# Performance work log

Hardware: AMD Instinct MI355X
Metric: run time of the kernel (lower is better)

Reference implementation:

```python
import jax, jax.numpy as jnp
import numpy as np

N_NODES = 50000
N_EDGES = 800000
NEG_SLOPE = 0.2


def _gat_layer(x, src, dst, W, a_src, a_dst, bias, heads, out_ch):
    """PyG-style GATConv with self-loops already appended to src/dst."""
    N = x.shape[0]
    h = (x @ W.T).reshape(N, heads, out_ch)            # [N,H,C]
    alpha_src = jnp.einsum('nhc,hc->nh', h, a_src)      # [N,H]
    alpha_dst = jnp.einsum('nhc,hc->nh', h, a_dst)      # [N,H]
    e = jax.nn.leaky_relu(alpha_src[src] + alpha_dst[dst], NEG_SLOPE)  # [E,H]
    # segment softmax over incoming edges of each destination node
    m = jax.ops.segment_max(e, dst, num_segments=N)     # [N,H]
    ex = jnp.exp(e - m[dst])
    denom = jax.ops.segment_sum(ex, dst, num_segments=N)  # [N,H] (>0: self-loops)
    alpha = ex / (denom[dst] + 1e-16)                    # [E,H]
    out = jax.ops.segment_sum(h[src] * alpha[:, :, None], dst, num_segments=N)  # [N,H,C]
    return out.reshape(N, heads * out_ch) + bias


def _with_self_loops(edge_index, n):
    loop = jnp.arange(n, dtype=edge_index.dtype)
    src = jnp.concatenate([edge_index[0], loop])
    dst = jnp.concatenate([edge_index[1], loop])
    return src, dst


def setup_inputs() -> dict:
    key = jax.random.key(0)
    ks = jax.random.split(key, 12)
    s = lambda fan: 1.0 / np.sqrt(fan)
    return {
        'x': jax.random.normal(ks[0], (N_NODES, 16), jnp.float32),
        'edge_index': jax.random.randint(ks[1], (2, N_EDGES), 0, N_NODES, jnp.int64),
        'W1': jax.random.normal(ks[2], (256, 16), jnp.float32) * s(16),
        'att_src1': jax.random.normal(ks[3], (4, 64), jnp.float32) * s(64),
        'att_dst1': jax.random.normal(ks[4], (4, 64), jnp.float32) * s(64),
        'b1': jnp.zeros((256,), jnp.float32),
        'W2': jax.random.normal(ks[5], (64, 256), jnp.float32) * s(256),
        'att_src2': jax.random.normal(ks[6], (1, 64), jnp.float32) * s(64),
        'att_dst2': jax.random.normal(ks[7], (1, 64), jnp.float32) * s(64),
        'b2': jnp.zeros((64,), jnp.float32),
        'fc_w': jax.random.normal(ks[8], (1, 64), jnp.float32) * s(64),
        'fc_b': jnp.zeros((1,), jnp.float32),
    }


def reference(x, edge_index, W1, att_src1, att_dst1, b1,
              W2, att_src2, att_dst2, b2, fc_w, fc_b):
    src, dst = _with_self_loops(edge_index, x.shape[0])
    h = jax.nn.elu(_gat_layer(x, src, dst, W1, att_src1, att_dst1, b1, heads=4, out_ch=64))
    h = jax.nn.elu(_gat_layer(h, src, dst, W2, att_src2, att_dst2, b2, heads=1, out_ch=64))
    return h @ fc_w.T + fc_b
```

## Files before the change

kernel.cpp:

```cpp
#include <hip/hip_runtime.h>
#include <hip/hip_bf16.h>
#include <stdint.h>

#define N_NODES 50000
#define N_EDGES 800000
#define MAXDEG  96
#define NSLICE  6250
#define NSB     196

#define OFF_X    0
#define OFF_W1   800000
#define OFF_AS1  804096
#define OFF_AD1  804352
#define OFF_B1   804608
#define OFF_W2   804864
#define OFF_AS2  821248
#define OFF_AD2  821312
#define OFF_B2   821376
#define OFF_FCW  821440
#define OFF_FCB  821504
#define N_CANON  821505
#define N_W2B    16384
#define N_W1B    16384
#define N_CONV   (N_CANON + N_W2B + N_W1B + N_NODES)

typedef __hip_bfloat16 bf16;
typedef __attribute__((ext_vector_type(8))) short short8;
typedef __attribute__((ext_vector_type(4))) float f32x4;

__device__ __forceinline__ float b2f(bf16 v){ return (float)v; }
__device__ __forceinline__ int clampi(int v, int lo, int hi){ return v < lo ? lo : (v > hi ? hi : v); }
__device__ __forceinline__ float clampf(float v){ return fminf(fmaxf(v, -40.f), 40.f); }
__device__ __forceinline__ uint16_t f2bfbits(float f){
  union { float f; uint32_t u; } c; c.f = f;
  uint32_t r = c.u + 0x7fff + ((c.u >> 16) & 1);
  return (uint16_t)(r >> 16);
}
__device__ __forceinline__ float bitsf(uint32_t u){
  union { uint32_t u; float f; } c; c.u = u; return c.f;
}
__device__ __forceinline__ uint32_t fbits(float f){
  union { float f; uint32_t u; } c; c.f = f; return c.u;
}

__device__ __forceinline__ int load_src(const int* ei, int i, int f){
  return f ? ei[2*(size_t)i] : ei[i];
}
__device__ __forceinline__ int load_dst(const int* ei, int i, int f){
  return f ? ei[2*((size_t)N_EDGES + i)] : ei[N_EDGES + i];
}

__global__ void k_detect(const int* __restrict__ ei, const uint16_t* __restrict__ xu,
                         int* __restrict__ flag){
  const int l = threadIdx.x;
  int or_odd = ei[2*l + 1] | ei[2*(400000 + l) + 1];
  int hits = 0;
  for(int k = 0; k < 64; k++){
    int e = (xu[l*64 + k] >> 7) & 0xFF;
    hits += (e >= 200);
  }
  #pragma unroll
  for(int off=32; off; off>>=1){
    or_odd |= __shfl_xor(or_odd, off, 64);
    hits   += __shfl_xor(hits,   off, 64);
  }
  if(l == 0){
    flag[0] = (or_odd == 0) ? 1 : 0;
    flag[1] = (hits > 16) ? 1 : 0;
  }
}

__global__ void k_convert(const void* x, const void* W1, const void* as1w, const void* ad1w,
                          const void* b1, const void* W2, const void* as2w, const void* ad2w,
                          const void* b2, const void* fcw, const void* fcb,
                          float* __restrict__ canon, uint16_t* __restrict__ W2b,
                          uint16_t* __restrict__ W1b, int* __restrict__ cnt,
                          int* __restrict__ csr_pad, const int* __restrict__ flag){
  int i = blockIdx.x*256 + threadIdx.x;
  int fp32 = flag[1];
  if(i >= N_CANON + N_W2B + N_W1B){
    int j = i - (N_CANON + N_W2B + N_W1B);
    if(j < N_NODES){ cnt[j] = 1; csr_pad[(size_t)j*MAXDEG] = j; }
    return;
  }
  if(i >= N_CANON + N_W2B){
    int j2 = i - (N_CANON + N_W2B);
    int j = j2 >> 6, kk = j2 & 63;
    uint16_t v = 0;
    if((kk >> 4) == (j >> 6)){
      int e = j*16 + (kk & 15);
      v = fp32 ? f2bfbits(((const float*)W1)[e]) : ((const uint16_t*)W1)[e];
    }
    W1b[j2] = v;
    return;
  }
  if(i >= N_CANON){
    int j = i - N_CANON;
    W2b[j] = fp32 ? f2bfbits(((const float*)W2)[j]) : ((const uint16_t*)W2)[j];
    return;
  }
  const void* src; int off;
  if     (i < OFF_W1 ){ src = x;    off = i; }
  else if(i < OFF_AS1){ src = W1;   off = i - OFF_W1; }
  else if(i < OFF_AD1){ src = as1w; off = i - OFF_AS1; }
  else if(i < OFF_B1 ){ src = ad1w; off = i - OFF_AD1; }
  else if(i < OFF_W2 ){ src = b1;   off = i - OFF_B1; }
  else if(i < OFF_AS2){ src = W2;   off = i - OFF_W2; }
  else if(i < OFF_AD2){ src = as2w; off = i - OFF_AS2; }
  else if(i < OFF_B2 ){ src = ad2w; off = i - OFF_AD2; }
  else if(i < OFF_FCW){ src = b2;   off = i - OFF_B2; }
  else if(i < OFF_FCB){ src = fcw;  off = i - OFF_FCW; }
  else               { src = fcb;  off = 0; }
  float v = fp32 ? ((const float*)src)[off] : b2f(((const bf16*)src)[off]);
  canon[i] = v;
}


__global__ __launch_bounds__(256) void k_prepscat(const float* __restrict__ canon,
                        uint32_t* __restrict__ pack, float* __restrict__ dpack,
                        const int* __restrict__ ei, int* __restrict__ cnt,
                        int* __restrict__ csr_pad, const int* __restrict__ flag){
  const int tid = threadIdx.x;
  if(blockIdx.x >= 196){
    const int bid = blockIdx.x - 196;
    const int grp = bid & 7, sb = bid >> 3;
    const int f = flag[0];
    const int lo = grp*NSLICE, hi = lo + NSLICE;
    const int base = sb*4096;
    #pragma unroll 4
    for(int j = 0; j < 16; j++){
      int i = base + j*256 + tid;
      if(i >= N_EDGES) break;
      int d = clampi(load_dst(ei, i, f), 0, N_NODES-1);
      if(d >= lo && d < hi){
        int s = clampi(load_src(ei, i, f), 0, N_NODES-1);
        int pos = atomicAdd(&cnt[d], 1);
        pos = clampi(pos, 0, MAXDEG-1);
        csr_pad[(size_t)d*MAXDEG + pos] = s;
      }
    }
    return;
  }
  __shared__ float ps[64], pd[64];
  if(tid < 128){
    int e = tid & 63;
    int h = e >> 4, k = e & 15;
    const float* av = canon + (tid < 64 ? OFF_AS1 : OFF_AD1) + h*64;
    const float* Wp = canon + OFF_W1 + (h*64)*16 + k;
    float acc = 0.f;
    #pragma unroll 8
    for(int c = 0; c < 64; c++) acc += av[c] * Wp[c*16];
    (tid < 64 ? ps : pd)[e] = acc;
  }
  __syncthreads();
  int n = blockIdx.x*256 + tid;
  if(n >= N_NODES) return;
  float xr[16];
  const float4* xp = (const float4*)(canon + OFF_X + n*16);
  #pragma unroll
  for(int t=0;t<4;t++){ float4 v = xp[t]; xr[4*t]=v.x; xr[4*t+1]=v.y; xr[4*t+2]=v.z; xr[4*t+3]=v.w; }
  uint32_t w[16];
  #pragma unroll
  for(int t=0;t<8;t++)
    w[t] = (uint32_t)f2bfbits(xr[2*t]) | ((uint32_t)f2bfbits(xr[2*t+1]) << 16);
  float qs[8];
  #pragma unroll
  for(int h=0;h<4;h++){
    float a=0.f, b=0.f;
    #pragma unroll
    for(int k=0;k<16;k++){ a += ps[h*16+k]*xr[k]; b += pd[h*16+k]*xr[k]; }
    a = clampf(a); b = clampf(b);
    w[8+2*h]  = fbits(__expf(a));
    w[9+2*h]  = fbits(__expf(0.2f*a));
    qs[2*h]   = __expf(b);
    qs[2*h+1] = __expf(0.2f*b);
  }
  uint4* dst = (uint4*)(pack + (size_t)n*16);
  dst[0] = make_uint4(w[0],w[1],w[2],w[3]);
  dst[1] = make_uint4(w[4],w[5],w[6],w[7]);
  dst[2] = make_uint4(w[8],w[9],w[10],w[11]);
  dst[3] = make_uint4(w[12],w[13],w[14],w[15]);
  float4* dd = (float4*)(dpack + (size_t)n*8);
  dd[0] = make_float4(qs[0],qs[1],qs[2],qs[3]);
  dd[1] = make_float4(qs[4],qs[5],qs[6],qs[7]);
}


struct Acc { float y0,y1,y2,y3,d0,d1,d2,d3; };

__device__ __forceinline__ void batch8(const int* __restrict__ csr, int i0, const char* pk,
                                       float2 qq, int g, int k, int h3, int base, Acc& a){
  int iA = csr[i0 + g], iB = csr[i0 + 4 + g];
  const char* rA = pk + (size_t)iA*64;
  const char* rB = pk + (size_t)iB*64;
  float xvA = bitsf((uint32_t)(*(const uint16_t*)(rA + k*2)) << 16);
  float2 ppA = *(const float2*)(rA + 32 + h3*8);
  float xvB = bitsf((uint32_t)(*(const uint16_t*)(rB + k*2)) << 16);
  float2 ppB = *(const float2*)(rB + 32 + h3*8);
  float wA = fmaxf(ppA.x*qq.x, ppA.y*qq.y);
  float wB = fmaxf(ppB.x*qq.x, ppB.y*qq.y);
  float a0 = __shfl(wA, base|0, 64), a1 = __shfl(wA, base|1, 64);
  float a2 = __shfl(wA, base|2, 64), a3 = __shfl(wA, base|3, 64);
  float b0 = __shfl(wB, base|0, 64), b1 = __shfl(wB, base|1, 64);
  float b2 = __shfl(wB, base|2, 64), b3 = __shfl(wB, base|3, 64);
  a.y0 += a0*xvA + b0*xvB; a.d0 += a0 + b0;
  a.y1 += a1*xvA + b1*xvB; a.d1 += a1 + b1;
  a.y2 += a2*xvA + b2*xvB; a.d2 += a2 + b2;
  a.y3 += a3*xvA + b3*xvB; a.d3 += a3 + b3;
}

__device__ __forceinline__ void tail8(const int* __restrict__ csr, int i0, int end, const char* pk,
                                      float2 qq, int g, int k, int h3, int base, Acc& a){
  int iiA = i0 + g, iiB = i0 + 4 + g;
  bool vA = iiA < end, vB = iiB < end;
  int iA = csr[vA ? iiA : end-1];
  int iB = csr[vB ? iiB : end-1];
  const char* rA = pk + (size_t)iA*64;
  const char* rB = pk + (size_t)iB*64;
  float xvA = bitsf((uint32_t)(*(const uint16_t*)(rA + k*2)) << 16);
  float2 ppA = *(const float2*)(rA + 32 + h3*8);
  float xvB = bitsf((uint32_t)(*(const uint16_t*)(rB + k*2)) << 16);
  float2 ppB = *(const float2*)(rB + 32 + h3*8);
  float wA = vA ? fmaxf(ppA.x*qq.x, ppA.y*qq.y) : 0.f;
  float wB = vB ? fmaxf(ppB.x*qq.x, ppB.y*qq.y) : 0.f;
  float a0 = __shfl(wA, base|0, 64), a1 = __shfl(wA, base|1, 64);
  float a2 = __shfl(wA, base|2, 64), a3 = __shfl(wA, base|3, 64);
  float b0 = __shfl(wB, base|0, 64), b1 = __shfl(wB, base|1, 64);
  float b2 = __shfl(wB, base|2, 64), b3 = __shfl(wB, base|3, 64);
  a.y0 += a0*xvA + b0*xvB; a.d0 += a0 + b0;
  a.y1 += a1*xvA + b1*xvB; a.d1 += a1 + b1;
  a.y2 += a2*xvA + b2*xvB; a.d2 += a2 + b2;
  a.y3 += a3*xvA + b3*xvB; a.d3 += a3 + b3;
}

__device__ __forceinline__ void store_y(Acc& a, int n, int g, int k, uint16_t* __restrict__ yb){
  a.y0 += __shfl_xor(a.y0,16,64); a.y0 += __shfl_xor(a.y0,32,64);
  a.y1 += __shfl_xor(a.y1,16,64); a.y1 += __shfl_xor(a.y1,32,64);
  a.y2 += __shfl_xor(a.y2,16,64); a.y2 += __shfl_xor(a.y2,32,64);
  a.y3 += __shfl_xor(a.y3,16,64); a.y3 += __shfl_xor(a.y3,32,64);
  a.d0 += __shfl_xor(a.d0,16,64); a.d0 += __shfl_xor(a.d0,32,64);
  a.d1 += __shfl_xor(a.d1,16,64); a.d1 += __shfl_xor(a.d1,32,64);
  a.d2 += __shfl_xor(a.d2,16,64); a.d2 += __shfl_xor(a.d2,32,64);
  a.d3 += __shfl_xor(a.d3,16,64); a.d3 += __shfl_xor(a.d3,32,64);
  float yH = (g==0) ? a.y0 : (g==1) ? a.y1 : (g==2) ? a.y2 : a.y3;
  float dH = (g==0) ? a.d0 : (g==1) ? a.d1 : (g==2) ? a.d2 : a.d3;
  yb[(size_t)n*64 + g*16 + k] = f2bfbits(yH / (dH + 1e-16f));
}

__global__ __launch_bounds__(256) void k_aggy(const int* __restrict__ cnt, const int* __restrict__ csr_pad,
                       const uint32_t* __restrict__ pack, const float* __restrict__ dpack,
                       uint16_t* __restrict__ yb){
  const int wv = threadIdx.x >> 6, lane = threadIdx.x & 63;
  const int g = lane >> 4, k = lane & 15, h3 = k & 3;
  const int base = lane & 48;
  const char* pk = (const char*)pack;

  for(int np = blockIdx.x*4 + wv; np < N_NODES/2; np += gridDim.x*4){
    const int nA = np*2, nB = np*2 + 1;
    const int begA = nA*MAXDEG, endA = begA + cnt[nA];
    const int begB = nB*MAXDEG, endB = begB + cnt[nB];
    const float2 qqA = *(const float2*)(dpack + (size_t)nA*8 + h3*2);
    const float2 qqB = *(const float2*)(dpack + (size_t)nB*8 + h3*2);
    Acc aA = {0,0,0,0,0,0,0,0}, aB = {0,0,0,0,0,0,0,0};
    int iA = begA, iB = begB;
    while(iA + 8 <= endA && iB + 8 <= endB){
      batch8(csr_pad, iA, pk, qqA, g, k, h3, base, aA);
      batch8(csr_pad, iB, pk, qqB, g, k, h3, base, aB);
      iA += 8; iB += 8;
    }
    while(iA + 8 <= endA){ batch8(csr_pad, iA, pk, qqA, g, k, h3, base, aA); iA += 8; }
    while(iB + 8 <= endB){ batch8(csr_pad, iB, pk, qqB, g, k, h3, base, aB); iB += 8; }
    if(iA < endA) tail8(csr_pad, iA, endA, pk, qqA, g, k, h3, base, aA);
    if(iB < endB) tail8(csr_pad, iB, endB, pk, qqB, g, k, h3, base, aB);
    store_y(aA, nA, g, k, yb);
    store_y(aB, nB, g, k, yb);
  }
}


__global__ __launch_bounds__(256) void k_h1(const uint16_t* __restrict__ yb,
                        const uint16_t* __restrict__ W1b, const float* __restrict__ canon,
                        bf16* __restrict__ h1o){
  const int tid = threadIdx.x, lane = tid & 63, wave = tid >> 6;
  const int quad = lane >> 4, c = lane & 15;

  short8 bfrag[16];
  float b1v[16];
  #pragma unroll
  for(int cb=0; cb<16; cb++){
    bfrag[cb] = *(const short8*)(W1b + (cb*16 + c)*64 + (cb>>3)*32 + quad*8);
    b1v[cb] = canon[OFF_B1 + cb*16 + c];
  }

  const int tiles = N_NODES/16;
  const int gw = blockIdx.x*4 + wave, nw = gridDim.x*4;
  for(int t = gw; t < tiles; t += nw){
    const int n0 = t*16;
    short8 af0 = *(const short8*)(yb + (size_t)(n0 + c)*64 + quad*8);
    short8 af1 = *(const short8*)(yb + (size_t)(n0 + c)*64 + 32 + quad*8);
    #pragma unroll
    for(int cb=0; cb<16; cb++){
      f32x4 acc = (f32x4){0.f,0.f,0.f,0.f};
      acc = __builtin_amdgcn_mfma_f32_16x16x32_bf16((cb>>3) ? af1 : af0, bfrag[cb], acc, 0,0,0);
      #pragma unroll
      for(int r=0; r<4; r++){
        float o = acc[r] + b1v[cb];
        o = (o > 0.f) ? o : expm1f(o);
        h1o[(size_t)(n0 + quad*4 + r)*256 + cb*16 + c] = __float2bfloat16(o);
      }
    }
  }
}


__global__ __launch_bounds__(256) void k_gemm2(const bf16* __restrict__ h1o, const uint16_t* __restrict__ W2b,
                        const float* __restrict__ canon,
                        bf16* __restrict__ h2, float2* __restrict__ pq2, float2* __restrict__ dq2){
  const int tid = threadIdx.x, lane = tid & 63, wave = tid >> 6;
  const int quad = lane >> 4, c = lane & 15;

  short8 bfrag[4][8];
  #pragma unroll
  for(int cb=0; cb<4; cb++)
    #pragma unroll
    for(int ks=0; ks<8; ks++)
      bfrag[cb][ks] = *(const short8*)(W2b + (cb*16 + c)*256 + ks*32 + quad*8);

  float asj[4], adj[4];
  #pragma unroll
  for(int cb=0; cb<4; cb++){
    asj[cb] = canon[OFF_AS2 + cb*16 + c];
    adj[cb] = canon[OFF_AD2 + cb*16 + c];
  }

  const int tiles = N_NODES/16;
  const int gw = blockIdx.x*4 + wave, nw = gridDim.x*4;
  for(int t = gw; t < tiles; t += nw){
    const int n0 = t*16;
    f32x4 acc[4];
    #pragma unroll
    for(int cb=0; cb<4; cb++) acc[cb] = (f32x4){0.f,0.f,0.f,0.f};

    const bf16* arow = h1o + (size_t)(n0 + c)*256 + quad*8;
    #pragma unroll
    for(int ks=0; ks<8; ks++){
      short8 af = *(const short8*)(arow + ks*32);
      acc[0] = __builtin_amdgcn_mfma_f32_16x16x32_bf16(af, bfrag[0][ks], acc[0], 0,0,0);
      acc[1] = __builtin_amdgcn_mfma_f32_16x16x32_bf16(af, bfrag[1][ks], acc[1], 0,0,0);
      acc[2] = __builtin_amdgcn_mfma_f32_16x16x32_bf16(af, bfrag[2][ks], acc[2], 0,0,0);
      acc[3] = __builtin_amdgcn_mfma_f32_16x16x32_bf16(af, bfrag[3][ks], acc[3], 0,0,0);
    }

    float vs[4] = {0.f,0.f,0.f,0.f}, vd[4] = {0.f,0.f,0.f,0.f};
    #pragma unroll
    for(int cb=0; cb<4; cb++)
      #pragma unroll
      for(int r=0; r<4; r++){
        float v = acc[cb][r];
        h2[(size_t)(n0 + quad*4 + r)*64 + cb*16 + c] = __float2bfloat16(v);
        vs[r] += v * asj[cb];
        vd[r] += v * adj[cb];
      }
    #pragma unroll
    for(int r=0; r<4; r++){
      #pragma unroll
      for(int off=1; off<16; off<<=1){
        vs[r] += __shfl_xor(vs[r], off, 64);
        vd[r] += __shfl_xor(vd[r], off, 64);
      }
    }
    if(c == 0){
      #pragma unroll
      for(int r=0; r<4; r++){
        float s = clampf(vs[r]), d = clampf(vd[r]);
        pq2[n0 + quad*4 + r] = make_float2(__expf(s), __expf(0.2f*s));
        dq2[n0 + quad*4 + r] = make_float2(__expf(d), __expf(0.2f*d));
      }
    }
  }
}


__global__ __launch_bounds__(256) void k_agg2(const int* __restrict__ cnt, const int* __restrict__ csr_pad,
                       const bf16* __restrict__ h2, const float2* __restrict__ pq2,
                       const float2* __restrict__ dq2, const float* __restrict__ canon,
                       void* __restrict__ outv, const int* __restrict__ flag){
  const int wv = threadIdx.x >> 6, lane = threadIdx.x & 63;
  const int g = lane >> 4, k = lane & 15;
  const char* h2b = (const char*)h2;
  float4 b2v = ((const float4*)(canon + OFF_B2))[k];
  float4 fcv = ((const float4*)(canon + OFF_FCW))[k];
  const float fcb0 = canon[OFF_FCB];
  const int ofp32 = flag[1];
  for(int n = blockIdx.x*4 + wv; n < N_NODES; n += gridDim.x*4){
    const int beg = n*MAXDEG, end = beg + cnt[n];
    const float2 qn = dq2[n];
    float a0=0.f,a1=0.f,a2=0.f,a3=0.f, den=0.f;
    int i0 = beg;
    const int nfull = (end - beg) >> 3;
    if(nfull > 0){
      int iA = csr_pad[i0 + g], iB = csr_pad[i0 + 4 + g];
      for(int b = 1; b < nfull; b++){
        int nA = csr_pad[i0 + 8 + g], nB = csr_pad[i0 + 12 + g];
        uint2 hA = *(const uint2*)(h2b + (size_t)iA*128 + k*8);
        float2 pA = pq2[iA];
        uint2 hB = *(const uint2*)(h2b + (size_t)iB*128 + k*8);
        float2 pB = pq2[iB];
        float wA = fmaxf(pA.x*qn.x, pA.y*qn.y);
        float wB = fmaxf(pB.x*qn.x, pB.y*qn.y);
        den += wA + wB;
        a0 += wA*bitsf(hA.x << 16) + wB*bitsf(hB.x << 16);
        a1 += wA*bitsf(hA.x & 0xffff0000u) + wB*bitsf(hB.x & 0xffff0000u);
        a2 += wA*bitsf(hA.y << 16) + wB*bitsf(hB.y << 16);
        a3 += wA*bitsf(hA.y & 0xffff0000u) + wB*bitsf(hB.y & 0xffff0000u);
        iA = nA; iB = nB;
        i0 += 8;
      }
      {
        uint2 hA = *(const uint2*)(h2b + (size_t)iA*128 + k*8);
        float2 pA = pq2[iA];
        uint2 hB = *(const uint2*)(h2b + (size_t)iB*128 + k*8);
        float2 pB = pq2[iB];
        float wA = fmaxf(pA.x*qn.x, pA.y*qn.y);
        float wB = fmaxf(pB.x*qn.x, pB.y*qn.y);
        den += wA + wB;
        a0 += wA*bitsf(hA.x << 16) + wB*bitsf(hB.x << 16);
        a1 += wA*bitsf(hA.x & 0xffff0000u) + wB*bitsf(hB.x & 0xffff0000u);
        a2 += wA*bitsf(hA.y << 16) + wB*bitsf(hB.y << 16);
        a3 += wA*bitsf(hA.y & 0xffff0000u) + wB*bitsf(hB.y & 0xffff0000u);
        i0 += 8;
      }
    }
    if(i0 < end){
      int iiA = i0 + g, iiB = i0 + 4 + g;
      bool vA = iiA < end, vB = iiB < end;
      int iA = csr_pad[vA ? iiA : end-1];
      int iB = csr_pad[vB ? iiB : end-1];
      uint2 hA = *(const uint2*)(h2b + (size_t)iA*128 + k*8);
      float2 pA = pq2[iA];
      uint2 hB = *(const uint2*)(h2b + (size_t)iB*128 + k*8);
      float2 pB = pq2[iB];
      float wA = vA ? fmaxf(pA.x*qn.x, pA.y*qn.y) : 0.f;
      float wB = vB ? fmaxf(pB.x*qn.x, pB.y*qn.y) : 0.f;
      den += wA + wB;
      a0 += wA*bitsf(hA.x << 16) + wB*bitsf(hB.x << 16);
      a1 += wA*bitsf(hA.x & 0xffff0000u) + wB*bitsf(hB.x & 0xffff0000u);
      a2 += wA*bitsf(hA.y << 16) + wB*bitsf(hB.y << 16);
      a3 += wA*bitsf(hA.y & 0xffff0000u) + wB*bitsf(hB.y & 0xffff0000u);
    }
    a0 += __shfl_xor(a0,16,64); a0 += __shfl_xor(a0,32,64);
    a1 += __shfl_xor(a1,16,64); a1 += __shfl_xor(a1,32,64);
    a2 += __shfl_xor(a2,16,64); a2 += __shfl_xor(a2,32,64);
    a3 += __shfl_xor(a3,16,64); a3 += __shfl_xor(a3,32,64);
    den += __shfl_xor(den,16,64); den += __shfl_xor(den,32,64);
    float inv = 1.f/(den + 1e-16f);
    float o0 = a0*inv + b2v.x, o1 = a1*inv + b2v.y;
    float o2 = a2*inv + b2v.z, o3 = a3*inv + b2v.w;
    o0 = (o0>0.f)?o0:expm1f(o0); o1 = (o1>0.f)?o1:expm1f(o1);
    o2 = (o2>0.f)?o2:expm1f(o2); o3 = (o3>0.f)?o3:expm1f(o3);
    float v = o0*fcv.x + o1*fcv.y + o2*fcv.z + o3*fcv.w;
    v += __shfl_xor(v,1,64); v += __shfl_xor(v,2,64);
    v += __shfl_xor(v,4,64); v += __shfl_xor(v,8,64);
    if(lane == 0){
      float r = v + fcb0;
      if(ofp32) ((float*)outv)[n] = r;
      else      ((bf16*)outv)[n] = __float2bfloat16(r);
    }
  }
}


extern "C" void kernel_launch(void* const* d_in, const int* in_sizes, int n_in,
                              void* d_out, int out_size, void* d_ws, size_t ws_size,
                              hipStream_t stream){
  (void)in_sizes; (void)n_in; (void)out_size;
  const int* ei = (const int*)d_in[1];

  char* w = (char*)d_ws;
  auto carve = [&](size_t bytes)->char*{ char* p = w; w += (bytes + 255) & ~(size_t)255; return p; };
  int*      cnt     = (int*)     carve((size_t)N_NODES*4);
  int*      flag    = (int*)     carve(256);
  int*      csr_pad = (int*)     carve((size_t)N_NODES*MAXDEG*4);
  float*    canon   = (float*)   carve((size_t)N_CANON*4);
  uint16_t* W2b     = (uint16_t*)carve((size_t)N_W2B*2);
  uint16_t* W1b     = (uint16_t*)carve((size_t)N_W1B*2);
  uint32_t* pack    = (uint32_t*)carve((size_t)N_NODES*64);
  float*    dpack   = (float*)   carve((size_t)N_NODES*32);
  uint16_t* yb      = (uint16_t*)carve((size_t)N_NODES*64*2);
  float2*   pq2     = (float2*)  carve((size_t)N_NODES*8);
  float2*   dq2     = (float2*)  carve((size_t)N_NODES*8);
  bf16*     h2      = (bf16*)    carve((size_t)N_NODES*64*2);
  bf16*     h1o     = (bf16*)    carve((size_t)N_NODES*256*2);
  size_t required = (size_t)(w - (char*)d_ws);
  if(ws_size < required) return;

  hipLaunchKernelGGL(k_detect,   dim3(1), dim3(64), 0, stream, ei, (const uint16_t*)d_in[0], flag);
  hipLaunchKernelGGL(k_convert,  dim3((N_CONV+255)/256), dim3(256), 0, stream,
                     d_in[0], d_in[2], d_in[3], d_in[4], d_in[5], d_in[6], d_in[7], d_in[8],
                     d_in[9], d_in[10], d_in[11], canon, W2b, W1b, cnt, csr_pad, flag);
  hipLaunchKernelGGL(k_prepscat, dim3(196 + 8*NSB), dim3(256), 0, stream,
                     canon, pack, dpack, ei, cnt, csr_pad, flag);
  hipLaunchKernelGGL(k_aggy,     dim3(2048), dim3(256), 0, stream, cnt, csr_pad, pack, dpack, yb);
  hipLaunchKernelGGL(k_h1,       dim3(782), dim3(256), 0, stream, yb, W1b, canon, h1o);
  hipLaunchKernelGGL(k_gemm2,    dim3(782), dim3(256), 0, stream, h1o, W2b, canon, h2, pq2, dq2);
  hipLaunchKernelGGL(k_agg2,     dim3(2048), dim3(256), 0, stream, cnt, csr_pad, h2, pq2, dq2, canon, d_out, flag);
}
```

Measured before the change: 221.1 us.

## Fuse layer-1 projection and layer-2 GEMM into one kernel via LDS tile

Merges k_h1 and k_gemm2 into a single k_mlp kernel. The 16x256 ELU'd h1 tile now stays in a per-wave LDS buffer with a padded stride instead of being written to and read back from a global 25.6 MB bf16 buffer. W1 fragments move from registers to LDS, which frees registers for the W2 fragments. This removes one launch and a large global round trip, at the cost of more LDS use per block (about 66 KB) and LDS bank traffic, which may limit occupancy.

```diff
diff --git a/kernel.cpp b/kernel.cpp
--- a/kernel.cpp
+++ b/kernel.cpp
@@ -23,6 +23,8 @@
 #define N_W2B    16384
 #define N_W1B    16384
 #define N_CONV   (N_CANON + N_W2B + N_W1B + N_NODES)
+
+#define TSTRIDE 264
 
 typedef __hip_bfloat16 bf16;
 typedef __attribute__((ext_vector_type(8))) short short8;
@@ -278,20 +280,40 @@
 }
 
 
-__global__ __launch_bounds__(256) void k_h1(const uint16_t* __restrict__ yb,
-                        const uint16_t* __restrict__ W1b, const float* __restrict__ canon,
-                        bf16* __restrict__ h1o){
+__global__ __launch_bounds__(256) void k_mlp(const uint16_t* __restrict__ yb,
+                        const uint16_t* __restrict__ W1b, const uint16_t* __restrict__ W2b,
+                        const float* __restrict__ canon,
+                        bf16* __restrict__ h2, float2* __restrict__ pq2, float2* __restrict__ dq2){
+  __shared__ uint16_t w1lds[N_W1B];
+  __shared__ uint16_t tile[4][16*TSTRIDE];
   const int tid = threadIdx.x, lane = tid & 63, wave = tid >> 6;
   const int quad = lane >> 4, c = lane & 15;
 
-  short8 bfrag[16];
+  {
+    const uint4* src = (const uint4*)W1b;
+    uint4* dst = (uint4*)w1lds;
+    for(int idx = tid; idx < N_W1B/8; idx += 256) dst[idx] = src[idx];
+  }
+  __syncthreads();
+
+  short8 bfrag[4][8];
+  #pragma unroll
+  for(int cb=0; cb<4; cb++)
+    #pragma unroll
+    for(int ks=0; ks<8; ks++)
+      bfrag[cb][ks] = *(const short8*)(W2b + (cb*16 + c)*256 + ks*32 + quad*8);
+
   float b1v[16];
   #pragma unroll
-  for(int cb=0; cb<16; cb++){
-    bfrag[cb] = *(const short8*)(W1b + (cb*16 + c)*64 + (cb>>3)*32 + quad*8);
-    b1v[cb] = canon[OFF_B1 + cb*16 + c];
-  }
-
+  for(int cb=0; cb<16; cb++) b1v[cb] = canon[OFF_B1 + cb*16 + c];
+  float asj[4], adj[4];
+  #pragma unroll
+  for(int cb=0; cb<4; cb++){
+    asj[cb] = canon[OFF_AS2 + cb*16 + c];
+    adj[cb] = canon[OFF_AD2 + cb*16 + c];
+  }
+
+  uint16_t* tl = tile[wave];
   const int tiles = N_NODES/16;
   const int gw = blockIdx.x*4 + wave, nw = gridDim.x*4;
   for(int t = gw; t < tiles; t += nw){
@@ -300,63 +322,33 @@
     short8 af1 = *(const short8*)(yb + (size_t)(n0 + c)*64 + 32 + quad*8);
     #pragma unroll
     for(int cb=0; cb<16; cb++){
+      short8 wf = *(const short8*)(w1lds + (cb*16 + c)*64 + (cb>>3)*32 + quad*8);
       f32x4 acc = (f32x4){0.f,0.f,0.f,0.f};
-      acc = __builtin_amdgcn_mfma_f32_16x16x32_bf16((cb>>3) ? af1 : af0, bfrag[cb], acc, 0,0,0);
+      acc = __builtin_amdgcn_mfma_f32_16x16x32_bf16((cb>>3) ? af1 : af0, wf, acc, 0,0,0);
       #pragma unroll
       for(int r=0; r<4; r++){
         float o = acc[r] + b1v[cb];
         o = (o > 0.f) ? o : expm1f(o);
-        h1o[(size_t)(n0 + quad*4 + r)*256 + cb*16 + c] = __float2bfloat16(o);
-      }
-    }
-  }
-}
-
-
-__global__ __launch_bounds__(256) void k_gemm2(const bf16* __restrict__ h1o, const uint16_t* __restrict__ W2b,
-                        const float* __restrict__ canon,
-                        bf16* __restrict__ h2, float2* __restrict__ pq2, float2* __restrict__ dq2){
-  const int tid = threadIdx.x, lane = tid & 63, wave = tid >> 6;
-  const int quad = lane >> 4, c = lane & 15;
-
-  short8 bfrag[4][8];
-  #pragma unroll
-  for(int cb=0; cb<4; cb++)
-    #pragma unroll
-    for(int ks=0; ks<8; ks++)
-      bfrag[cb][ks] = *(const short8*)(W2b + (cb*16 + c)*256 + ks*32 + quad*8);
-
-  float asj[4], adj[4];
-  #pragma unroll
-  for(int cb=0; cb<4; cb++){
-    asj[cb] = canon[OFF_AS2 + cb*16 + c];
-    adj[cb] = canon[OFF_AD2 + cb*16 + c];
-  }
-
-  const int tiles = N_NODES/16;
-  const int gw = blockIdx.x*4 + wave, nw = gridDim.x*4;
-  for(int t = gw; t < tiles; t += nw){
-    const int n0 = t*16;
-    f32x4 acc[4];
-    #pragma unroll
-    for(int cb=0; cb<4; cb++) acc[cb] = (f32x4){0.f,0.f,0.f,0.f};
-
-    const bf16* arow = h1o + (size_t)(n0 + c)*256 + quad*8;
+        tl[(quad*4 + r)*TSTRIDE + cb*16 + c] = f2bfbits(o);
+      }
+    }
+    f32x4 acc2[4];
+    #pragma unroll
+    for(int cb=0; cb<4; cb++) acc2[cb] = (f32x4){0.f,0.f,0.f,0.f};
     #pragma unroll
     for(int ks=0; ks<8; ks++){
-      short8 af = *(const short8*)(arow + ks*32);
-      acc[0] = __builtin_amdgcn_mfma_f32_16x16x32_bf16(af, bfrag[0][ks], acc[0], 0,0,0);
-      acc[1] = __builtin_amdgcn_mfma_f32_16x16x32_bf16(af, bfrag[1][ks], acc[1], 0,0,0);
-      acc[2] = __builtin_amdgcn_mfma_f32_16x16x32_bf16(af, bfrag[2][ks], acc[2], 0,0,0);
-      acc[3] = __builtin_amdgcn_mfma_f32_16x16x32_bf16(af, bfrag[3][ks], acc[3], 0,0,0);
-    }
-
+      short8 af = *(const short8*)(tl + c*TSTRIDE + ks*32 + quad*8);
+      acc2[0] = __builtin_amdgcn_mfma_f32_16x16x32_bf16(af, bfrag[0][ks], acc2[0], 0,0,0);
+      acc2[1] = __builtin_amdgcn_mfma_f32_16x16x32_bf16(af, bfrag[1][ks], acc2[1], 0,0,0);
+      acc2[2] = __builtin_amdgcn_mfma_f32_16x16x32_bf16(af, bfrag[2][ks], acc2[2], 0,0,0);
+      acc2[3] = __builtin_amdgcn_mfma_f32_16x16x32_bf16(af, bfrag[3][ks], acc2[3], 0,0,0);
+    }
     float vs[4] = {0.f,0.f,0.f,0.f}, vd[4] = {0.f,0.f,0.f,0.f};
     #pragma unroll
     for(int cb=0; cb<4; cb++)
       #pragma unroll
       for(int r=0; r<4; r++){
-        float v = acc[cb][r];
+        float v = acc2[cb][r];
         h2[(size_t)(n0 + quad*4 + r)*64 + cb*16 + c] = __float2bfloat16(v);
         vs[r] += v * asj[cb];
         vd[r] += v * adj[cb];
@@ -490,7 +482,6 @@
   float2*   pq2     = (float2*)  carve((size_t)N_NODES*8);
   float2*   dq2     = (float2*)  carve((size_t)N_NODES*8);
   bf16*     h2      = (bf16*)    carve((size_t)N_NODES*64*2);
-  bf16*     h1o     = (bf16*)    carve((size_t)N_NODES*256*2);
   size_t required = (size_t)(w - (char*)d_ws);
   if(ws_size < required) return;
 
@@ -501,7 +492,6 @@
   hipLaunchKernelGGL(k_prepscat, dim3(196 + 8*NSB), dim3(256), 0, stream,
                      canon, pack, dpack, ei, cnt, csr_pad, flag);
   hipLaunchKernelGGL(k_aggy,     dim3(2048), dim3(256), 0, stream, cnt, csr_pad, pack, dpack, yb);
-  hipLaunchKernelGGL(k_h1,       dim3(782), dim3(256), 0, stream, yb, W1b, canon, h1o);
-  hipLaunchKernelGGL(k_gemm2,    dim3(782), dim3(256), 0, stream, h1o, W2b, canon, h2, pq2, dq2);
+  hipLaunchKernelGGL(k_mlp,      dim3(782), dim3(256), 0, stream, yb, W1b, W2b, canon, h2, pq2, dq2);
   hipLaunchKernelGGL(k_agg2,     dim3(2048), dim3(256), 0, stream, cnt, csr_pad, h2, pq2, dq2, canon, d_out, flag);
 }
```

Measured after the change: 211.4 us, median of 2. 4.4% less time.
